# Optimization experiments

Hardware: AMD Instinct MI355X
Metric: run time of the kernel (lower is better)

Reference implementation:

```python
import jax, jax.numpy as jnp
import numpy as np

N_HEAD = 16

def setup_inputs() -> dict:
    key = jax.random.key(0)
    kx, kq, kk, kv, kp = jax.random.split(key, 5)
    B, T, C = 4, 2048, 1024
    scale = 1.0 / np.sqrt(C)
    x = jax.random.normal(kx, (B, T, C), dtype=jnp.float32)
    Wq = jax.random.normal(kq, (C, C), dtype=jnp.float32) * scale
    Wk = jax.random.normal(kk, (C, C), dtype=jnp.float32) * scale
    Wv = jax.random.normal(kv, (C, C), dtype=jnp.float32) * scale
    Wp = jax.random.normal(kp, (C, C), dtype=jnp.float32) * scale
    return {"x": x, "Wq": Wq, "Wk": Wk, "Wv": Wv, "Wp": Wp}

def reference(x, Wq, Wk, Wv, Wp):
    B, T, C = x.shape
    H = N_HEAD
    D = C // H
    # projections (nn.Linear, no bias): x @ W^T
    q = (x @ Wq.T).reshape(B, T, H, D).transpose(0, 2, 1, 3)  # [B,H,T,D]
    k = (x @ Wk.T).reshape(B, T, H, D).transpose(0, 2, 1, 3)
    v = (x @ Wv.T).reshape(B, T, H, D).transpose(0, 2, 1, 3)
    att = jnp.einsum('bhqd,bhkd->bhqk', q, k) / jnp.sqrt(jnp.float32(D))
    causal = jnp.tril(jnp.ones((T, T), dtype=bool))
    att = jnp.where(causal, att, -jnp.inf)
    att = jax.nn.softmax(att, axis=-1)
    # dropout p=0.0 -> identity
    y = jnp.einsum('bhqk,bhkd->bhqd', att, v)  # [B,H,T,D]
    y = y.transpose(0, 2, 1, 3).reshape(B, T, C)
    return y @ Wp.T
```

## Files before the change

kernel.cpp:

```cpp
#include <hip/hip_runtime.h>

typedef __bf16 bfrag __attribute__((ext_vector_type(8)));
typedef __bf16 bh4 __attribute__((ext_vector_type(4)));
typedef float f4 __attribute__((ext_vector_type(4)));

#define AS1C(p) (const __attribute__((address_space(1))) void*)(p)
#define AS3(p)  (__attribute__((address_space(3))) void*)(p)

#define QSCALE 0.18033688011112042f

__device__ __forceinline__ void g2l16(const __bf16* g, __bf16* l) {
  __builtin_amdgcn_global_load_lds(AS1C(g), AS3(l), 16, 0, 0);
}

__global__ __launch_bounds__(256) void cvt5(
    const float* __restrict__ s0, const float* __restrict__ s1,
    const float* __restrict__ s2, const float* __restrict__ s3,
    const float* __restrict__ s4,
    __bf16* __restrict__ d0, __bf16* __restrict__ d1, __bf16* __restrict__ d2,
    __bf16* __restrict__ d3, __bf16* __restrict__ d4, long n0, long n1) {
  const float* s; __bf16* d; long n;
  switch (blockIdx.y) {
    case 0: s = s0; d = d0; n = n0; break;
    case 1: s = s1; d = d1; n = n1; break;
    case 2: s = s2; d = d2; n = n1; break;
    case 3: s = s3; d = d3; n = n1; break;
    default: s = s4; d = d4; n = n1; break;
  }
  long i = ((long)blockIdx.x * 256 + threadIdx.x) * 8;
  if (i >= n) return;
  float4 a = *(const float4*)(s + i);
  float4 b = *(const float4*)(s + i + 4);
  bfrag o;
  o[0] = (__bf16)a.x; o[1] = (__bf16)a.y; o[2] = (__bf16)a.z; o[3] = (__bf16)a.w;
  o[4] = (__bf16)b.x; o[5] = (__bf16)b.y; o[6] = (__bf16)b.z; o[7] = (__bf16)b.w;
  *(bfrag*)(d + i) = o;
}

__global__ __launch_bounds__(256) void gemm_qkv(
    const __bf16* __restrict__ A, const __bf16* __restrict__ B,
    __bf16* __restrict__ qb, __bf16* __restrict__ kb, __bf16* __restrict__ vt,
    int M, int K) {
  __shared__ __bf16 sbuf[16640];
  __bf16* As0 = sbuf;
  __bf16* As1 = sbuf + 4096;
  __bf16* Bs0 = sbuf + 8192;
  __bf16* Bs1 = sbuf + 12288;
  const int tid = threadIdx.x;
  const int wave = tid >> 6, lane = tid & 63;
  const int lm = lane & 15, quad = lane >> 4;
  const int bm = blockIdx.x * 128, bn = blockIdx.y * 128;
  const int wr = (wave >> 1) * 64, wc = (wave & 1) * 64;
  f4 acc[4][4] = {};
  for (int k0 = 0; k0 < K; k0 += 64) {
#pragma unroll
    for (int ii = 0; ii < 2; ++ii) {
      int s = ii * 4 + wave;
      int e = s * 512 + lane * 8;
      int r = e >> 5, c = e & 31;
      const __bf16* ar = A + (long)(bm + r) * K + k0 + c;
      const __bf16* br = B + (long)(bn + r) * K + k0 + c;
      g2l16(ar, As0 + e);
      g2l16(ar + 32, As1 + e);
      g2l16(br, Bs0 + e);
      g2l16(br + 32, Bs1 + e);
    }
    __syncthreads();
#pragma unroll
    for (int st = 0; st < 2; ++st) {
      const __bf16* As = st ? As1 : As0;
      const __bf16* Bs = st ? Bs1 : Bs0;
      bfrag af[4], bg[4];
#pragma unroll
      for (int mi = 0; mi < 4; ++mi)
        af[mi] = *(const bfrag*)(As + (wr + mi * 16 + lm) * 32 + quad * 8);
#pragma unroll
      for (int ni = 0; ni < 4; ++ni)
        bg[ni] = *(const bfrag*)(Bs + (wc + ni * 16 + lm) * 32 + quad * 8);
#pragma unroll
      for (int mi = 0; mi < 4; ++mi)
#pragma unroll
        for (int ni = 0; ni < 4; ++ni)
          acc[mi][ni] = __builtin_amdgcn_mfma_f32_16x16x32_bf16(af[mi], bg[ni], acc[mi][ni], 0, 0, 0);
    }
    __syncthreads();
  }
  if (bn < 2048) {
    __bf16* dst = (bn < 1024) ? qb : kb;
    const float scl = (bn < 1024) ? QSCALE : 1.0f;
    const int nb = bn & 1023;
#pragma unroll
    for (int mi = 0; mi < 4; ++mi)
#pragma unroll
      for (int ni = 0; ni < 4; ++ni)
#pragma unroll
        for (int r = 0; r < 4; ++r) {
          long row = bm + wr + mi * 16 + quad * 4 + r;
          long col = nb + wc + ni * 16 + lm;
          dst[row * 1024 + col] = (__bf16)(acc[mi][ni][r] * scl);
        }
  } else {
#pragma unroll
    for (int mi = 0; mi < 4; ++mi)
#pragma unroll
      for (int ni = 0; ni < 4; ++ni)
#pragma unroll
        for (int r = 0; r < 4; ++r) {
          int d = wc + ni * 16 + lm;
          int tp = (wr ? 64 : 0) + (quad * 4 + r) * 4 + mi;
          sbuf[d * 130 + tp] = (__bf16)acc[mi][ni][r];
        }
    __syncthreads();
    const int bloc = bm >> 11;
    const int tloc = bm & 2047;
#pragma unroll
    for (int p = 0; p < 8; ++p) {
      int d = (tid >> 4) + p * 16;
      int c = (tid & 15) * 8;
      long dglob = (bn - 2048) + d;
      *(bfrag*)(vt + ((long)bloc * 1024 + dglob) * 2048 + tloc + c) =
          *(const bfrag*)(sbuf + d * 130 + c);
    }
  }
}

template <bool OUT_F32>
__global__ __launch_bounds__(256) void gemm_bt_bf16(
    const __bf16* __restrict__ A, const __bf16* __restrict__ B,
    void* __restrict__ Cp, int M, int N, int K) {
  __shared__ __bf16 sbuf[16384];
  __bf16* As0 = sbuf;
  __bf16* As1 = sbuf + 4096;
  __bf16* Bs0 = sbuf + 8192;
  __bf16* Bs1 = sbuf + 12288;
  const int tid = threadIdx.x;
  const int wave = tid >> 6, lane = tid & 63;
  const int lm = lane & 15, quad = lane >> 4;
  const int bm = blockIdx.x * 128, bn = blockIdx.y * 128;
  const int wr = (wave >> 1) * 64, wc = (wave & 1) * 64;
  f4 acc[4][4] = {};
  for (int k0 = 0; k0 < K; k0 += 64) {
#pragma unroll
    for (int ii = 0; ii < 2; ++ii) {
      int s = ii * 4 + wave;
      int e = s * 512 + lane * 8;
      int r = e >> 5, c = e & 31;
      const __bf16* ar = A + (long)(bm + r) * K + k0 + c;
      const __bf16* br = B + (long)(bn + r) * K + k0 + c;
      g2l16(ar, As0 + e);
      g2l16(ar + 32, As1 + e);
      g2l16(br, Bs0 + e);
      g2l16(br + 32, Bs1 + e);
    }
    __syncthreads();
#pragma unroll
    for (int st = 0; st < 2; ++st) {
      const __bf16* As = st ? As1 : As0;
      const __bf16* Bs = st ? Bs1 : Bs0;
      bfrag af[4], bg[4];
#pragma unroll
      for (int mi = 0; mi < 4; ++mi)
        af[mi] = *(const bfrag*)(As + (wr + mi * 16 + lm) * 32 + quad * 8);
#pragma unroll
      for (int ni = 0; ni < 4; ++ni)
        bg[ni] = *(const bfrag*)(Bs + (wc + ni * 16 + lm) * 32 + quad * 8);
#pragma unroll
      for (int mi = 0; mi < 4; ++mi)
#pragma unroll
        for (int ni = 0; ni < 4; ++ni)
          acc[mi][ni] = __builtin_amdgcn_mfma_f32_16x16x32_bf16(af[mi], bg[ni], acc[mi][ni], 0, 0, 0);
    }
    __syncthreads();
  }
#pragma unroll
  for (int mi = 0; mi < 4; ++mi)
#pragma unroll
    for (int ni = 0; ni < 4; ++ni)
#pragma unroll
      for (int r = 0; r < 4; ++r) {
        long row = bm + wr + mi * 16 + quad * 4 + r;
        long col = bn + wc + ni * 16 + lm;
        if (OUT_F32) ((float*)Cp)[row * N + col] = acc[mi][ni][r];
        else ((__bf16*)Cp)[row * N + col] = (__bf16)acc[mi][ni][r];
      }
}

template <bool A_F32, bool OUT_F32>
__global__ __launch_bounds__(256) void gemm_bt_cv(
    const void* __restrict__ Ap, const float* __restrict__ Bp,
    void* __restrict__ Cp, int M, int N, int K, float scl) {
  __shared__ __bf16 As[128 * 32];
  __shared__ __bf16 Bs[128 * 32];
  const int tid = threadIdx.x;
  const int lane = tid & 63, wave = tid >> 6;
  const int lm = lane & 15, quad = lane >> 4;
  const int bm = blockIdx.x * 128, bn = blockIdx.y * 128;
  const int wr = (wave >> 1) * 64, wc = (wave & 1) * 64;
  const int e0 = tid * 16, sr = e0 >> 5, sc = e0 & 31;
  f4 acc[4][4] = {};
  for (int k0 = 0; k0 < K; k0 += 32) {
    if (A_F32) {
      const float4* ga = (const float4*)((const float*)Ap + (long)(bm + sr) * K + k0 + sc);
#pragma unroll
      for (int j = 0; j < 4; ++j) {
        float4 v = ga[j];
        As[sr * 32 + sc + j * 4 + 0] = (__bf16)v.x;
        As[sr * 32 + sc + j * 4 + 1] = (__bf16)v.y;
        As[sr * 32 + sc + j * 4 + 2] = (__bf16)v.z;
        As[sr * 32 + sc + j * 4 + 3] = (__bf16)v.w;
      }
    } else {
      const __bf16* Ab = (const __bf16*)Ap + (long)(bm + sr) * K + k0 + sc;
      *(bfrag*)(As + sr * 32 + sc) = *(const bfrag*)Ab;
      *(bfrag*)(As + sr * 32 + sc + 8) = *(const bfrag*)(Ab + 8);
    }
    {
      const float4* gb = (const float4*)(Bp + (long)(bn + sr) * K + k0 + sc);
#pragma unroll
      for (int j = 0; j < 4; ++j) {
        float4 v = gb[j];
        Bs[sr * 32 + sc + j * 4 + 0] = (__bf16)v.x;
        Bs[sr * 32 + sc + j * 4 + 1] = (__bf16)v.y;
        Bs[sr * 32 + sc + j * 4 + 2] = (__bf16)v.z;
        Bs[sr * 32 + sc + j * 4 + 3] = (__bf16)v.w;
      }
    }
    __syncthreads();
    bfrag af[4], bg[4];
#pragma unroll
    for (int mi = 0; mi < 4; ++mi)
      af[mi] = *(const bfrag*)(As + (wr + mi * 16 + lm) * 32 + quad * 8);
#pragma unroll
    for (int ni = 0; ni < 4; ++ni)
      bg[ni] = *(const bfrag*)(Bs + (wc + ni * 16 + lm) * 32 + quad * 8);
#pragma unroll
    for (int mi = 0; mi < 4; ++mi)
#pragma unroll
      for (int ni = 0; ni < 4; ++ni)
        acc[mi][ni] = __builtin_amdgcn_mfma_f32_16x16x32_bf16(af[mi], bg[ni], acc[mi][ni], 0, 0, 0);
    __syncthreads();
  }
#pragma unroll
  for (int mi = 0; mi < 4; ++mi)
#pragma unroll
    for (int ni = 0; ni < 4; ++ni)
#pragma unroll
      for (int r = 0; r < 4; ++r) {
        long row = bm + wr + mi * 16 + quad * 4 + r;
        long col = bn + wc + ni * 16 + lm;
        if (OUT_F32) ((float*)Cp)[row * N + col] = acc[mi][ni][r] * scl;
        else ((__bf16*)Cp)[row * N + col] = (__bf16)(acc[mi][ni][r] * scl);
      }
}

#define KP 72

template <bool VT>
__global__ __launch_bounds__(256, 2) void attn_fwd8(
    const __bf16* Qg, const __bf16* __restrict__ Kg,
    const __bf16* __restrict__ Vsrc, __bf16* Yg) {
  const int TT = 2048, CC = 1024;
  __shared__ __bf16 Ks[64 * KP];
  __shared__ __bf16 Vs[64 * KP];
  __shared__ __bf16 Ps[16 * 16 * KP];
  const int tid = threadIdx.x;
  const int wave = tid >> 6, lane = tid & 63;
  const int lm = lane & 15, quad = lane >> 4;
  const int bh = blockIdx.x, i = blockIdx.y;
  const int b = bh >> 4, h = bh & 15;
  const int qtA = i, qtB = 15 - i;
  const long rbase = (long)b * TT;
  const int hoff = h * 64;
  int row0[4];
  row0[0] = qtA * 128 + wave * 16;
  row0[1] = qtA * 128 + 64 + wave * 16;
  row0[2] = qtB * 128 + wave * 16;
  row0[3] = qtB * 128 + 64 + wave * 16;
  __bf16* Pw[4];
#pragma unroll
  for (int fr = 0; fr < 4; ++fr) Pw[fr] = Ps + (wave * 4 + fr) * 16 * KP;
  bfrag qf[4][2];
#pragma unroll
  for (int fr = 0; fr < 4; ++fr)
#pragma unroll
    for (int f = 0; f < 2; ++f)
      qf[fr][f] = *(const bfrag*)(Qg + (rbase + row0[fr] + lm) * CC + hoff + f * 32 + quad * 8);
  bfrag ones;
#pragma unroll
  for (int j = 0; j < 8; ++j) ones[j] = (__bf16)1.0f;
  f4 y[4][4] = {};
  f4 L[4] = {};

  const int ktLast = 2 * qtB + 1;
  bfrag kin[2], vin[2];
#pragma unroll
  for (int s = 0; s < 2; ++s) {
    int idx = tid + s * 256;
    int r = idx >> 3, c = (idx & 7) * 8;
    kin[s] = *(const bfrag*)(Kg + (rbase + r) * CC + hoff + c);
    if (VT)
      vin[s] = *(const bfrag*)(Vsrc + ((long)b * 1024 + hoff + r) * 2048 + c);
    else
      vin[s] = *(const bfrag*)(Vsrc + (rbase + r) * CC + hoff + c);
  }

  for (int kt = 0; kt <= ktLast; ++kt) {
    const int kBase = kt * 64;
    __syncthreads();
#pragma unroll
    for (int s = 0; s < 2; ++s) {
      int idx = tid + s * 256;
      int r = idx >> 3, c = (idx & 7) * 8;
      *(bfrag*)(Ks + r * KP + c) = kin[s];
      if (VT) {
        *(bfrag*)(Vs + r * KP + c) = vin[s];
      } else {
        int kp = (r & 15) * 4 + (r >> 4);
#pragma unroll
        for (int j = 0; j < 8; ++j) Vs[(c + j) * KP + kp] = vin[s][j];
      }
    }
    const bool more = (kt < ktLast);
    bfrag kin2[2], vin2[2];
    if (more) {
      const int nB = kBase + 64;
#pragma unroll
      for (int s = 0; s < 2; ++s) {
        int idx = tid + s * 256;
        int r = idx >> 3, c = (idx & 7) * 8;
        kin2[s] = *(const bfrag*)(Kg + (rbase + nB + r) * CC + hoff + c);
        if (VT)
          vin2[s] = *(const bfrag*)(Vsrc + ((long)b * 1024 + hoff + r) * 2048 + nB + c);
        else
          vin2[s] = *(const bfrag*)(Vsrc + (rbase + nB + r) * CC + hoff + c);
      }
    }
    __syncthreads();
    bfrag kf[8];
#pragma unroll
    for (int sub = 0; sub < 4; ++sub)
#pragma unroll
      for (int f = 0; f < 2; ++f)
        kf[sub * 2 + f] = *(const bfrag*)(Ks + (sub * 16 + lm) * KP + f * 32 + quad * 8);
#pragma unroll
    for (int fr = 0; fr < 4; ++fr) {
      if (kBase <= row0[fr] + 15) {
        f4 sac[4];
#pragma unroll
        for (int sub = 0; sub < 4; ++sub) {
          f4 z = {};
#pragma unroll
          for (int f = 0; f < 2; ++f)
            z = __builtin_amdgcn_mfma_f32_16x16x32_bf16(qf[fr][f], kf[sub * 2 + f], z, 0, 0, 0);
          sac[sub] = z;
        }
        if (kBase + 63 > row0[fr]) {
#pragma unroll
          for (int r = 0; r < 4; ++r) {
            bh4 pk;
#pragma unroll
            for (int sub = 0; sub < 4; ++sub) {
              float pv = __builtin_amdgcn_exp2f(sac[sub][r]);
              bool masked = (kBase + sub * 16 + lm > row0[fr] + quad * 4 + r);
              pk[sub] = (__bf16)(masked ? 0.f : pv);
            }
            *(bh4*)(Pw[fr] + (quad * 4 + r) * KP + lm * 4) = pk;
          }
        } else {
#pragma unroll
          for (int r = 0; r < 4; ++r) {
            bh4 pk;
#pragma unroll
            for (int sub = 0; sub < 4; ++sub)
              pk[sub] = (__bf16)__builtin_amdgcn_exp2f(sac[sub][r]);
            *(bh4*)(Pw[fr] + (quad * 4 + r) * KP + lm * 4) = pk;
          }
        }
      }
    }
    __asm__ volatile("s_waitcnt lgkmcnt(0)" ::: "memory");
    bfrag vf[8];
#pragma unroll
    for (int sub = 0; sub < 4; ++sub)
#pragma unroll
      for (int f = 0; f < 2; ++f)
        vf[sub * 2 + f] = *(const bfrag*)(Vs + (sub * 16 + lm) * KP + f * 32 + quad * 8);
#pragma unroll
    for (int fr = 0; fr < 4; ++fr) {
      if (kBase <= row0[fr] + 15) {
#pragma unroll
        for (int f = 0; f < 2; ++f) {
          bfrag pf = *(const bfrag*)(Pw[fr] + lm * KP + f * 32 + quad * 8);
          L[fr] = __builtin_amdgcn_mfma_f32_16x16x32_bf16(pf, ones, L[fr], 0, 0, 0);
#pragma unroll
          for (int ds = 0; ds < 4; ++ds)
            y[fr][ds] = __builtin_amdgcn_mfma_f32_16x16x32_bf16(pf, vf[ds * 2 + f], y[fr][ds], 0, 0, 0);
        }
      }
    }
    if (more) {
      kin[0] = kin2[0]; kin[1] = kin2[1];
      vin[0] = vin2[0]; vin[1] = vin2[1];
    }
  }
#pragma unroll
  for (int fr = 0; fr < 4; ++fr)
#pragma unroll
    for (int ds = 0; ds < 4; ++ds)
#pragma unroll
      for (int r = 0; r < 4; ++r) {
        long row = rbase + row0[fr] + quad * 4 + r;
        Yg[row * CC + hoff + ds * 16 + lm] = (__bf16)(y[fr][ds][r] / L[fr][r]);
      }
}

extern "C" void kernel_launch(void* const* d_in, const int* in_sizes, int n_in,
                              void* d_out, int out_size, void* d_ws, size_t ws_size,
                              hipStream_t stream) {
  (void)in_sizes; (void)n_in; (void)out_size;
  const float* x  = (const float*)d_in[0];
  const float* Wq = (const float*)d_in[1];
  const float* Wk = (const float*)d_in[2];
  const float* Wv = (const float*)d_in[3];
  const float* Wp = (const float*)d_in[4];
  float* out = (float*)d_out;
  const long R = 8192;
  const long BUF = R * 1024;
  const long WN = 1024L * 1024;
  __bf16* qb = (__bf16*)d_ws;
  __bf16* kb = (__bf16*)d_out;
  __bf16* vslot = kb + BUF;
  dim3 blk(256, 1, 1);
  const size_t need = (size_t)(2 * BUF + 4 * WN) * 2;
  if (ws_size >= need) {
    __bf16* xb = qb + BUF;
    __bf16* wqkv = xb + BUF;
    __bf16* wpb = wqkv + 3 * WN;
    cvt5<<<dim3((unsigned)(BUF / (256 * 8)), 5, 1), blk, 0, stream>>>(
        x, Wq, Wk, Wv, Wp, xb, wqkv, wqkv + WN, wqkv + 2 * WN, wpb, BUF, WN);
    gemm_qkv<<<dim3(64, 24, 1), blk, 0, stream>>>(xb, wqkv, qb, kb, vslot, 8192, 1024);
    attn_fwd8<true><<<dim3(64, 8, 1), blk, 0, stream>>>(qb, kb, vslot, qb);
    gemm_bt_bf16<true><<<dim3(64, 8, 1), blk, 0, stream>>>(qb, wpb, out, 8192, 1024, 1024);
  } else {
    gemm_bt_cv<true, false><<<dim3(64, 8, 1), blk, 0, stream>>>(x, Wq, qb, 8192, 1024, 1024, QSCALE);
    gemm_bt_cv<true, false><<<dim3(64, 8, 1), blk, 0, stream>>>(x, Wk, kb, 8192, 1024, 1024, 1.0f);
    gemm_bt_cv<true, false><<<dim3(64, 8, 1), blk, 0, stream>>>(x, Wv, vslot, 8192, 1024, 1024, 1.0f);
    attn_fwd8<false><<<dim3(64, 8, 1), blk, 0, stream>>>(qb, kb, vslot, qb);
    gemm_bt_cv<false, true><<<dim3(64, 8, 1), blk, 0, stream>>>(qb, Wp, out, 8192, 1024, 1024, 1.0f);
  }
}
```

Measured before the change: 229.2 us.

## Rewrite QKV projection GEMM as 256x256 tile, 8-wave pipelined kernel with swizzled LDS

Replaces the 128x128 QKV GEMM with a 512-thread, 256x256-tile kernel. It double-buffers A and B tiles through a swizzled 128 KB LDS region and interleaves async global-to-LDS staging with MFMA phases separated by barriers. The goals are more data reuse per tile, hidden load latency and fewer LDS bank conflicts. It also adds s_setprio around MFMA blocks in the attention kernel and changes the grid of the unused fallback attention launch. The costs are heavy register pressure from the 8x4 accumulators, and with 128 KB of LDS per block occupancy is limited to one block per CU.

Result: no change. 232.8 us (+1.6%).

```diff
diff --git a/kernel.cpp b/kernel.cpp
--- a/kernel.cpp
+++ b/kernel.cpp
@@ -37,89 +37,149 @@
   *(bfrag*)(d + i) = o;
 }
 
-__global__ __launch_bounds__(256) void gemm_qkv(
-    const __bf16* __restrict__ A, const __bf16* __restrict__ B,
-    __bf16* __restrict__ qb, __bf16* __restrict__ kb, __bf16* __restrict__ vt,
-    int M, int K) {
-  __shared__ __bf16 sbuf[16640];
-  __bf16* As0 = sbuf;
-  __bf16* As1 = sbuf + 4096;
-  __bf16* Bs0 = sbuf + 8192;
-  __bf16* Bs1 = sbuf + 12288;
+#define BARR __builtin_amdgcn_s_barrier()
+#define WAIT_LGKM { asm volatile("s_waitcnt lgkmcnt(0)" ::: "memory"); \
+                    __builtin_amdgcn_sched_barrier(0); }
+#define WAIT_VM(N) asm volatile("s_waitcnt vmcnt(" #N ")" ::: "memory")
+
+__global__ __launch_bounds__(512, 2) void gemm_qkv8(
+    const __bf16* __restrict__ A, const __bf16* __restrict__ Bw,
+    __bf16* __restrict__ qb, __bf16* __restrict__ kb,
+    __bf16* __restrict__ vt, int K) {
+  __shared__ __bf16 lds[65536];
   const int tid = threadIdx.x;
   const int wave = tid >> 6, lane = tid & 63;
   const int lm = lane & 15, quad = lane >> 4;
-  const int bm = blockIdx.x * 128, bn = blockIdx.y * 128;
-  const int wr = (wave >> 1) * 64, wc = (wave & 1) * 64;
-  f4 acc[4][4] = {};
-  for (int k0 = 0; k0 < K; k0 += 64) {
-#pragma unroll
-    for (int ii = 0; ii < 2; ++ii) {
-      int s = ii * 4 + wave;
-      int e = s * 512 + lane * 8;
-      int r = e >> 5, c = e & 31;
-      const __bf16* ar = A + (long)(bm + r) * K + k0 + c;
-      const __bf16* br = B + (long)(bn + r) * K + k0 + c;
-      g2l16(ar, As0 + e);
-      g2l16(ar + 32, As1 + e);
-      g2l16(br, Bs0 + e);
-      g2l16(br + 32, Bs1 + e);
-    }
-    __syncthreads();
-#pragma unroll
-    for (int st = 0; st < 2; ++st) {
-      const __bf16* As = st ? As1 : As0;
-      const __bf16* Bs = st ? Bs1 : Bs0;
-      bfrag af[4], bg[4];
-#pragma unroll
-      for (int mi = 0; mi < 4; ++mi)
-        af[mi] = *(const bfrag*)(As + (wr + mi * 16 + lm) * 32 + quad * 8);
-#pragma unroll
-      for (int ni = 0; ni < 4; ++ni)
-        bg[ni] = *(const bfrag*)(Bs + (wc + ni * 16 + lm) * 32 + quad * 8);
-#pragma unroll
-      for (int mi = 0; mi < 4; ++mi)
-#pragma unroll
-        for (int ni = 0; ni < 4; ++ni)
-          acc[mi][ni] = __builtin_amdgcn_mfma_f32_16x16x32_bf16(af[mi], bg[ni], acc[mi][ni], 0, 0, 0);
-    }
-    __syncthreads();
-  }
+  const int wm = wave >> 2, wn = wave & 3;
+  const int bm = blockIdx.x * 256, bn = blockIdx.y * 256;
+  const int srow = lane >> 3;
+  const int scol = ((lane & 7) ^ srow) * 8;
+  const int rsw = lm & 7;
+
+#define STG_A(bb, kt, h) { \
+    const __bf16* gp_ = A + (long)(bm + (h)*128 + wave*16 + srow) * K + (kt)*64 + scol; \
+    __bf16* lp_ = lds + (bb)*16384 + (h)*8192 + wave*1024 + lane*8; \
+    g2l16(gp_, lp_); g2l16(gp_ + 8*K, lp_ + 512); }
+#define STG_B(bb, kt, h) { \
+    const __bf16* gp_ = Bw + (long)(bn + (h)*128 + wave*16 + srow) * K + (kt)*64 + scol; \
+    __bf16* lp_ = lds + 32768 + (bb)*16384 + (h)*8192 + wave*1024 + lane*8; \
+    g2l16(gp_, lp_); g2l16(gp_ + 8*K, lp_ + 512); }
+
+#define LDA(dst, bb, mh) { \
+    const __bf16* base_ = lds + (bb)*16384 + (wm*128 + (mh)*64 + lm) * 64; \
+    _Pragma("unroll") for (int j_ = 0; j_ < 4; ++j_) \
+      _Pragma("unroll") for (int kk_ = 0; kk_ < 2; ++kk_) \
+        dst[j_][kk_] = *(const bfrag*)(base_ + j_*1024 + ((kk_*4 + quad) ^ rsw) * 8); }
+#define LDB(dst, bb, nh) { \
+    const __bf16* base_ = lds + 32768 + (bb)*16384 + (wn*64 + (nh)*32 + lm) * 64; \
+    _Pragma("unroll") for (int n_ = 0; n_ < 2; ++n_) \
+      _Pragma("unroll") for (int kk_ = 0; kk_ < 2; ++kk_) \
+        dst[n_][kk_] = *(const bfrag*)(base_ + n_*1024 + ((kk_*4 + quad) ^ rsw) * 8); }
+
+#define MM(MH, NH, BG) { \
+    __builtin_amdgcn_s_setprio(1); \
+    _Pragma("unroll") for (int j_ = 0; j_ < 4; ++j_) \
+      _Pragma("unroll") for (int n_ = 0; n_ < 2; ++n_) \
+        _Pragma("unroll") for (int kk_ = 0; kk_ < 2; ++kk_) \
+          acc[(MH)*4 + j_][(NH)*2 + n_] = __builtin_amdgcn_mfma_f32_16x16x32_bf16( \
+              af[j_][kk_], BG[n_][kk_], acc[(MH)*4 + j_][(NH)*2 + n_], 0, 0, 0); \
+    __builtin_amdgcn_s_setprio(0); }
+
+  f4 acc[8][4] = {};
+  bfrag af[4][2], bgA[2][2], bgB[2][2];
+
+  STG_A(0, 0, 0); STG_A(0, 0, 1); STG_B(0, 0, 0); STG_B(0, 0, 1);
+  STG_B(1, 1, 0); STG_B(1, 1, 1);
+  WAIT_VM(4);
+  BARR;
+
+  const int niter = K >> 7;
+#pragma unroll 1
+  for (int i = 0; i < niter; ++i) {
+    const bool last = (i == niter - 1);
+    const int o = 2 * i + 1, e2 = 2 * i + 2, o2 = 2 * i + 3;
+    LDA(af, 0, 0); LDB(bgA, 0, 0);
+    STG_A(1, o, 0);
+    BARR; WAIT_LGKM;
+    MM(0, 0, bgA);
+    BARR;
+    LDB(bgB, 0, 1);
+    STG_A(1, o, 1);
+    BARR; WAIT_LGKM;
+    MM(0, 1, bgB);
+    BARR;
+    LDA(af, 0, 1);
+    if (!last) STG_B(0, e2, 0);
+    BARR; WAIT_LGKM;
+    MM(1, 1, bgB);
+    BARR;
+    if (!last) STG_B(0, e2, 1);
+    BARR; WAIT_LGKM;
+    MM(1, 0, bgA);
+    if (last) { WAIT_VM(0); } else { WAIT_VM(4); }
+    BARR;
+    LDA(af, 1, 0); LDB(bgA, 1, 0);
+    if (!last) STG_A(0, e2, 0);
+    BARR; WAIT_LGKM;
+    MM(0, 0, bgA);
+    BARR;
+    LDB(bgB, 1, 1);
+    if (!last) STG_A(0, e2, 1);
+    BARR; WAIT_LGKM;
+    MM(0, 1, bgB);
+    BARR;
+    LDA(af, 1, 1);
+    if (!last) STG_B(1, o2, 0);
+    BARR; WAIT_LGKM;
+    MM(1, 1, bgB);
+    BARR;
+    if (!last) STG_B(1, o2, 1);
+    BARR; WAIT_LGKM;
+    MM(1, 0, bgA);
+    if (!last) WAIT_VM(4);
+    BARR;
+  }
+
   if (bn < 2048) {
     __bf16* dst = (bn < 1024) ? qb : kb;
     const float scl = (bn < 1024) ? QSCALE : 1.0f;
     const int nb = bn & 1023;
 #pragma unroll
-    for (int mi = 0; mi < 4; ++mi)
+    for (int mi = 0; mi < 8; ++mi)
 #pragma unroll
       for (int ni = 0; ni < 4; ++ni)
 #pragma unroll
         for (int r = 0; r < 4; ++r) {
-          long row = bm + wr + mi * 16 + quad * 4 + r;
-          long col = nb + wc + ni * 16 + lm;
+          long row = bm + wm * 128 + mi * 16 + quad * 4 + r;
+          long col = nb + wn * 64 + ni * 16 + lm;
           dst[row * 1024 + col] = (__bf16)(acc[mi][ni][r] * scl);
         }
   } else {
-#pragma unroll
-    for (int mi = 0; mi < 4; ++mi)
-#pragma unroll
-      for (int ni = 0; ni < 4; ++ni)
-#pragma unroll
-        for (int r = 0; r < 4; ++r) {
-          int d = wc + ni * 16 + lm;
-          int tp = (wr ? 64 : 0) + (quad * 4 + r) * 4 + mi;
-          sbuf[d * 130 + tp] = (__bf16)acc[mi][ni][r];
-        }
-    __syncthreads();
     const int bloc = bm >> 11;
     const int tloc = bm & 2047;
 #pragma unroll
-    for (int p = 0; p < 8; ++p) {
-      int d = (tid >> 4) + p * 16;
-      int c = (tid & 15) * 8;
-      long dglob = (bn - 2048) + d;
-      *(bfrag*)(vt + ((long)bloc * 1024 + dglob) * 2048 + tloc + c) =
-          *(const bfrag*)(sbuf + d * 130 + c);
+    for (int h = 0; h < 2; ++h) {
+      if (wm == h) {
+#pragma unroll
+        for (int mi = 0; mi < 8; ++mi)
+#pragma unroll
+          for (int ni = 0; ni < 4; ++ni)
+#pragma unroll
+            for (int r = 0; r < 4; ++r) {
+              int d = wn * 64 + ni * 16 + lm;
+              int tp = (mi >> 2) * 64 + (quad * 4 + r) * 4 + (mi & 3);
+              lds[d * 130 + tp] = (__bf16)acc[mi][ni][r];
+            }
+      }
+      __syncthreads();
+#pragma unroll
+      for (int p = 0; p < 8; ++p) {
+        int d = (tid >> 4) + p * 32;
+        int c = (tid & 15) * 8;
+        *(bfrag*)(vt + ((long)bloc * 1024 + (bn - 2048) + d) * 2048 + tloc + h * 128 + c) =
+            *(const bfrag*)(lds + d * 130 + c);
+      }
+      __syncthreads();
     }
   }
 }
@@ -346,6 +406,7 @@
     for (int fr = 0; fr < 4; ++fr) {
       if (kBase <= row0[fr] + 15) {
         f4 sac[4];
+        __builtin_amdgcn_s_setprio(1);
 #pragma unroll
         for (int sub = 0; sub < 4; ++sub) {
           f4 z = {};
@@ -354,6 +415,7 @@
             z = __builtin_amdgcn_mfma_f32_16x16x32_bf16(qf[fr][f], kf[sub * 2 + f], z, 0, 0, 0);
           sac[sub] = z;
         }
+        __builtin_amdgcn_s_setprio(0);
         if (kBase + 63 > row0[fr]) {
 #pragma unroll
           for (int r = 0; r < 4; ++r) {
@@ -388,6 +450,7 @@
 #pragma unroll
     for (int fr = 0; fr < 4; ++fr) {
       if (kBase <= row0[fr] + 15) {
+        __builtin_amdgcn_s_setprio(1);
 #pragma unroll
         for (int f = 0; f < 2; ++f) {
           bfrag pf = *(const bfrag*)(Pw[fr] + lm * KP + f * 32 + quad * 8);
@@ -396,6 +459,7 @@
           for (int ds = 0; ds < 4; ++ds)
             y[fr][ds] = __builtin_amdgcn_mfma_f32_16x16x32_bf16(pf, vf[ds * 2 + f], y[fr][ds], 0, 0, 0);
         }
+        __builtin_amdgcn_s_setprio(0);
       }
     }
     if (more) {
@@ -438,14 +502,14 @@
     __bf16* wpb = wqkv + 3 * WN;
     cvt5<<<dim3((unsigned)(BUF / (256 * 8)), 5, 1), blk, 0, stream>>>(
         x, Wq, Wk, Wv, Wp, xb, wqkv, wqkv + WN, wqkv + 2 * WN, wpb, BUF, WN);
-    gemm_qkv<<<dim3(64, 24, 1), blk, 0, stream>>>(xb, wqkv, qb, kb, vslot, 8192, 1024);
+    gemm_qkv8<<<dim3(32, 12, 1), dim3(512, 1, 1), 0, stream>>>(xb, wqkv, qb, kb, vslot, 1024);
     attn_fwd8<true><<<dim3(64, 8, 1), blk, 0, stream>>>(qb, kb, vslot, qb);
     gemm_bt_bf16<true><<<dim3(64, 8, 1), blk, 0, stream>>>(qb, wpb, out, 8192, 1024, 1024);
   } else {
     gemm_bt_cv<true, false><<<dim3(64, 8, 1), blk, 0, stream>>>(x, Wq, qb, 8192, 1024, 1024, QSCALE);
     gemm_bt_cv<true, false><<<dim3(64, 8, 1), blk, 0, stream>>>(x, Wk, kb, 8192, 1024, 1024, 1.0f);
     gemm_bt_cv<true, false><<<dim3(64, 8, 1), blk, 0, stream>>>(x, Wv, vslot, 8192, 1024, 1024, 1.0f);
-    attn_fwd8<false><<<dim3(64, 8, 1), blk, 0, stream>>>(qb, kb, vslot, qb);
+    attn_fwd8<false><<<dim3(16, 64, 1), blk, 0, stream>>>(qb, kb, vslot, qb);
     gemm_bt_cv<false, true><<<dim3(64, 8, 1), blk, 0, stream>>>(qb, Wp, out, 8192, 1024, 1024, 1.0f);
   }
 }
```

## Replace projection GEMMs with triple-buffered swizzled 128x256 tile kernel

Applied to the files above, without the earlier changes.

Replaces the QKV and output-projection GEMM kernels with one templated 512-thread kernel. It uses 128x256 block tiles, a three-stage LDS ring filled by global_load_lds, and XOR-swizzled LDS layout to avoid bank conflicts. It also uses explicit vmcnt/lgkmcnt waits, raw barriers and s_setprio around MFMA bursts. The goal is to overlap global loads with MFMA work and cut LDS conflicts and barrier stalls. The cost is a large LDS footprint that limits occupancy to one block per CU, and manual wait counts that must match the number of issued loads.

Measured after the change: 227.4 us. About the same (-0.8%).

```diff
diff --git a/kernel.cpp b/kernel.cpp
--- a/kernel.cpp
+++ b/kernel.cpp
@@ -37,55 +37,100 @@
   *(bfrag*)(d + i) = o;
 }
 
-__global__ __launch_bounds__(256) void gemm_qkv(
-    const __bf16* __restrict__ A, const __bf16* __restrict__ B,
-    __bf16* __restrict__ qb, __bf16* __restrict__ kb, __bf16* __restrict__ vt,
-    int M, int K) {
-  __shared__ __bf16 sbuf[16640];
-  __bf16* As0 = sbuf;
-  __bf16* As1 = sbuf + 4096;
-  __bf16* Bs0 = sbuf + 8192;
-  __bf16* Bs1 = sbuf + 12288;
+#define BARR __builtin_amdgcn_s_barrier()
+#define WAIT_LGKM { asm volatile("s_waitcnt lgkmcnt(0)" ::: "memory"); \
+                    __builtin_amdgcn_sched_barrier(0); }
+#define WAIT_VM(N) asm volatile("s_waitcnt vmcnt(" #N ")" ::: "memory")
+
+template <int MODE>
+__global__ __launch_bounds__(512, 2) void gemm_dp(
+    const __bf16* __restrict__ A, const __bf16* __restrict__ Bw,
+    __bf16* __restrict__ qb, __bf16* __restrict__ kb,
+    __bf16* __restrict__ vt, float* __restrict__ Cf, int K) {
+  __shared__ __bf16 lds[73728];
+  __bf16* ldsA = lds;
+  __bf16* ldsB = lds + 24576;
   const int tid = threadIdx.x;
   const int wave = tid >> 6, lane = tid & 63;
   const int lm = lane & 15, quad = lane >> 4;
-  const int bm = blockIdx.x * 128, bn = blockIdx.y * 128;
-  const int wr = (wave >> 1) * 64, wc = (wave & 1) * 64;
+  const int wm = wave >> 2, wn = wave & 3;
+  const int bm = blockIdx.x * 128, bn = blockIdx.y * 256;
+  const int srow = lane >> 3;
+  const int scol = ((lane & 7) ^ srow) * 8;
+  const int rsw = lm & 7;
+
+#define STG_A9(sl, kt) { \
+    const __bf16* gp_ = A + (long)(bm + wave * 16 + srow) * K + (kt) * 64 + scol; \
+    __bf16* lp_ = ldsA + (sl) * 8192 + wave * 1024 + lane * 8; \
+    g2l16(gp_, lp_); g2l16(gp_ + 8 * K, lp_ + 512); }
+#define STG_B9(sl, kt, h) { \
+    const __bf16* gp_ = Bw + (long)(bn + (h) * 128 + wave * 16 + srow) * K + (kt) * 64 + scol; \
+    __bf16* lp_ = ldsB + (sl) * 16384 + (h) * 8192 + wave * 1024 + lane * 8; \
+    g2l16(gp_, lp_); g2l16(gp_ + 8 * K, lp_ + 512); }
+#define STG_TILE(sl, kt) { STG_A9(sl, kt); STG_B9(sl, kt, 0); STG_B9(sl, kt, 1); }
+
+#define COMPUTE_HALF(sl) { \
+    const __bf16* Ab_ = ldsA + (sl) * 8192 + (wm * 64 + lm) * 64; \
+    const __bf16* Bb_ = ldsB + (sl) * 16384 + (wn * 64 + lm) * 64; \
+    bfrag af_[4][2], bg_[2][2]; \
+    _Pragma("unroll") for (int j_ = 0; j_ < 4; ++j_) \
+      _Pragma("unroll") for (int kk_ = 0; kk_ < 2; ++kk_) \
+        af_[j_][kk_] = *(const bfrag*)(Ab_ + j_ * 1024 + ((kk_ * 4 + quad) ^ rsw) * 8); \
+    _Pragma("unroll") for (int n_ = 0; n_ < 2; ++n_) \
+      _Pragma("unroll") for (int kk_ = 0; kk_ < 2; ++kk_) \
+        bg_[n_][kk_] = *(const bfrag*)(Bb_ + n_ * 1024 + ((kk_ * 4 + quad) ^ rsw) * 8); \
+    WAIT_LGKM; \
+    __builtin_amdgcn_s_setprio(1); \
+    _Pragma("unroll") for (int j_ = 0; j_ < 4; ++j_) \
+      _Pragma("unroll") for (int n_ = 0; n_ < 2; ++n_) \
+        _Pragma("unroll") for (int kk_ = 0; kk_ < 2; ++kk_) \
+          acc[j_][n_] = __builtin_amdgcn_mfma_f32_16x16x32_bf16( \
+              af_[j_][kk_], bg_[n_][kk_], acc[j_][n_], 0, 0, 0); \
+    __builtin_amdgcn_s_setprio(0); \
+    _Pragma("unroll") for (int n_ = 0; n_ < 2; ++n_) \
+      _Pragma("unroll") for (int kk_ = 0; kk_ < 2; ++kk_) \
+        bg_[n_][kk_] = *(const bfrag*)(Bb_ + (2 + n_) * 1024 + ((kk_ * 4 + quad) ^ rsw) * 8); \
+    WAIT_LGKM; \
+    __builtin_amdgcn_s_setprio(1); \
+    _Pragma("unroll") for (int j_ = 0; j_ < 4; ++j_) \
+      _Pragma("unroll") for (int n_ = 0; n_ < 2; ++n_) \
+        _Pragma("unroll") for (int kk_ = 0; kk_ < 2; ++kk_) \
+          acc[j_][2 + n_] = __builtin_amdgcn_mfma_f32_16x16x32_bf16( \
+              af_[j_][kk_], bg_[n_][kk_], acc[j_][2 + n_], 0, 0, 0); \
+    __builtin_amdgcn_s_setprio(0); }
+
   f4 acc[4][4] = {};
-  for (int k0 = 0; k0 < K; k0 += 64) {
-#pragma unroll
-    for (int ii = 0; ii < 2; ++ii) {
-      int s = ii * 4 + wave;
-      int e = s * 512 + lane * 8;
-      int r = e >> 5, c = e & 31;
-      const __bf16* ar = A + (long)(bm + r) * K + k0 + c;
-      const __bf16* br = B + (long)(bn + r) * K + k0 + c;
-      g2l16(ar, As0 + e);
-      g2l16(ar + 32, As1 + e);
-      g2l16(br, Bs0 + e);
-      g2l16(br + 32, Bs1 + e);
-    }
-    __syncthreads();
-#pragma unroll
-    for (int st = 0; st < 2; ++st) {
-      const __bf16* As = st ? As1 : As0;
-      const __bf16* Bs = st ? Bs1 : Bs0;
-      bfrag af[4], bg[4];
-#pragma unroll
-      for (int mi = 0; mi < 4; ++mi)
-        af[mi] = *(const bfrag*)(As + (wr + mi * 16 + lm) * 32 + quad * 8);
+  const int ntiles = K >> 6;
+  STG_TILE(0, 0);
+  STG_TILE(1, 1);
+  WAIT_VM(6);
+  BARR;
+#pragma unroll 1
+  for (int i = 0; i < (ntiles >> 1); ++i) {
+    const int e = 2 * i, o = 2 * i + 1;
+    const int se = e % 3, so = o % 3;
+    if (e + 2 < ntiles) { const int s2 = (e + 2) % 3; STG_TILE(s2, e + 2); }
+    COMPUTE_HALF(se);
+    if (e + 2 < ntiles) { WAIT_VM(6); } else { WAIT_VM(0); }
+    BARR;
+    if (o + 2 < ntiles) { const int s2 = (o + 2) % 3; STG_TILE(s2, o + 2); }
+    COMPUTE_HALF(so);
+    if (o + 2 < ntiles) WAIT_VM(6);
+    BARR;
+  }
+
+  if (MODE == 1) {
+#pragma unroll
+    for (int mi = 0; mi < 4; ++mi)
 #pragma unroll
       for (int ni = 0; ni < 4; ++ni)
-        bg[ni] = *(const bfrag*)(Bs + (wc + ni * 16 + lm) * 32 + quad * 8);
-#pragma unroll
-      for (int mi = 0; mi < 4; ++mi)
-#pragma unroll
-        for (int ni = 0; ni < 4; ++ni)
-          acc[mi][ni] = __builtin_amdgcn_mfma_f32_16x16x32_bf16(af[mi], bg[ni], acc[mi][ni], 0, 0, 0);
-    }
-    __syncthreads();
-  }
-  if (bn < 2048) {
+#pragma unroll
+        for (int r = 0; r < 4; ++r) {
+          long row = bm + wm * 64 + mi * 16 + quad * 4 + r;
+          long col = bn + wn * 64 + ni * 16 + lm;
+          Cf[row * 1024 + col] = acc[mi][ni][r];
+        }
+  } else if (bn < 2048) {
     __bf16* dst = (bn < 1024) ? qb : kb;
     const float scl = (bn < 1024) ? QSCALE : 1.0f;
     const int nb = bn & 1023;
@@ -95,8 +140,8 @@
       for (int ni = 0; ni < 4; ++ni)
 #pragma unroll
         for (int r = 0; r < 4; ++r) {
-          long row = bm + wr + mi * 16 + quad * 4 + r;
-          long col = nb + wc + ni * 16 + lm;
+          long row = bm + wm * 64 + mi * 16 + quad * 4 + r;
+          long col = nb + wn * 64 + ni * 16 + lm;
           dst[row * 1024 + col] = (__bf16)(acc[mi][ni][r] * scl);
         }
   } else {
@@ -106,83 +151,22 @@
       for (int ni = 0; ni < 4; ++ni)
 #pragma unroll
         for (int r = 0; r < 4; ++r) {
-          int d = wc + ni * 16 + lm;
-          int tp = (wr ? 64 : 0) + (quad * 4 + r) * 4 + mi;
-          sbuf[d * 130 + tp] = (__bf16)acc[mi][ni][r];
+          int d = wn * 64 + ni * 16 + lm;
+          int tp = wm * 64 + (quad * 4 + r) * 4 + mi;
+          lds[d * 130 + tp] = (__bf16)acc[mi][ni][r];
         }
     __syncthreads();
     const int bloc = bm >> 11;
     const int tloc = bm & 2047;
 #pragma unroll
     for (int p = 0; p < 8; ++p) {
-      int d = (tid >> 4) + p * 16;
+      int d = (tid >> 4) + p * 32;
       int c = (tid & 15) * 8;
       long dglob = (bn - 2048) + d;
       *(bfrag*)(vt + ((long)bloc * 1024 + dglob) * 2048 + tloc + c) =
-          *(const bfrag*)(sbuf + d * 130 + c);
-    }
-  }
-}
-
-template <bool OUT_F32>
-__global__ __launch_bounds__(256) void gemm_bt_bf16(
-    const __bf16* __restrict__ A, const __bf16* __restrict__ B,
-    void* __restrict__ Cp, int M, int N, int K) {
-  __shared__ __bf16 sbuf[16384];
-  __bf16* As0 = sbuf;
-  __bf16* As1 = sbuf + 4096;
-  __bf16* Bs0 = sbuf + 8192;
-  __bf16* Bs1 = sbuf + 12288;
-  const int tid = threadIdx.x;
-  const int wave = tid >> 6, lane = tid & 63;
-  const int lm = lane & 15, quad = lane >> 4;
-  const int bm = blockIdx.x * 128, bn = blockIdx.y * 128;
-  const int wr = (wave >> 1) * 64, wc = (wave & 1) * 64;
-  f4 acc[4][4] = {};
-  for (int k0 = 0; k0 < K; k0 += 64) {
-#pragma unroll
-    for (int ii = 0; ii < 2; ++ii) {
-      int s = ii * 4 + wave;
-      int e = s * 512 + lane * 8;
-      int r = e >> 5, c = e & 31;
-      const __bf16* ar = A + (long)(bm + r) * K + k0 + c;
-      const __bf16* br = B + (long)(bn + r) * K + k0 + c;
-      g2l16(ar, As0 + e);
-      g2l16(ar + 32, As1 + e);
-      g2l16(br, Bs0 + e);
-      g2l16(br + 32, Bs1 + e);
-    }
-    __syncthreads();
-#pragma unroll
-    for (int st = 0; st < 2; ++st) {
-      const __bf16* As = st ? As1 : As0;
-      const __bf16* Bs = st ? Bs1 : Bs0;
-      bfrag af[4], bg[4];
-#pragma unroll
-      for (int mi = 0; mi < 4; ++mi)
-        af[mi] = *(const bfrag*)(As + (wr + mi * 16 + lm) * 32 + quad * 8);
-#pragma unroll
-      for (int ni = 0; ni < 4; ++ni)
-        bg[ni] = *(const bfrag*)(Bs + (wc + ni * 16 + lm) * 32 + quad * 8);
-#pragma unroll
-      for (int mi = 0; mi < 4; ++mi)
-#pragma unroll
-        for (int ni = 0; ni < 4; ++ni)
-          acc[mi][ni] = __builtin_amdgcn_mfma_f32_16x16x32_bf16(af[mi], bg[ni], acc[mi][ni], 0, 0, 0);
-    }
-    __syncthreads();
-  }
-#pragma unroll
-  for (int mi = 0; mi < 4; ++mi)
-#pragma unroll
-    for (int ni = 0; ni < 4; ++ni)
-#pragma unroll
-      for (int r = 0; r < 4; ++r) {
-        long row = bm + wr + mi * 16 + quad * 4 + r;
-        long col = bn + wc + ni * 16 + lm;
-        if (OUT_F32) ((float*)Cp)[row * N + col] = acc[mi][ni][r];
-        else ((__bf16*)Cp)[row * N + col] = (__bf16)acc[mi][ni][r];
-      }
+          *(const bfrag*)(lds + d * 130 + c);
+    }
+  }
 }
 
 template <bool A_F32, bool OUT_F32>
@@ -438,9 +422,11 @@
     __bf16* wpb = wqkv + 3 * WN;
     cvt5<<<dim3((unsigned)(BUF / (256 * 8)), 5, 1), blk, 0, stream>>>(
         x, Wq, Wk, Wv, Wp, xb, wqkv, wqkv + WN, wqkv + 2 * WN, wpb, BUF, WN);
-    gemm_qkv<<<dim3(64, 24, 1), blk, 0, stream>>>(xb, wqkv, qb, kb, vslot, 8192, 1024);
+    gemm_dp<0><<<dim3(64, 12, 1), dim3(512, 1, 1), 0, stream>>>(
+        xb, wqkv, qb, kb, vslot, nullptr, 1024);
     attn_fwd8<true><<<dim3(64, 8, 1), blk, 0, stream>>>(qb, kb, vslot, qb);
-    gemm_bt_bf16<true><<<dim3(64, 8, 1), blk, 0, stream>>>(qb, wpb, out, 8192, 1024, 1024);
+    gemm_dp<1><<<dim3(64, 4, 1), dim3(512, 1, 1), 0, stream>>>(
+        qb, wpb, nullptr, nullptr, nullptr, out, 1024);
   } else {
     gemm_bt_cv<true, false><<<dim3(64, 8, 1), blk, 0, stream>>>(x, Wq, qb, 8192, 1024, 1024, QSCALE);
     gemm_bt_cv<true, false><<<dim3(64, 8, 1), blk, 0, stream>>>(x, Wk, kb, 8192, 1024, 1024, 1.0f);
```
